# Kernel optimization log

Hardware: AMD Instinct MI355X
Metric: run time of the kernel (lower is better)

## Reference

```python
import jax, jax.numpy as jnp
import numpy as np

# Performer config (from module __init__):
# dim=768, depth=4, heads=12, dim_head=64, nb_features=64,
# generalized_attention=True with ReLU kernel, reversible=True,
# ff_mult=4, shift_tokens=True (shifts=(-1,0,1) since causal=False),
# qkv_bias=True, attn_out_bias=True, ff_chunks=1, dropout=0.
L, D, H, DH, M = 4, 768, 12, 64, 64
FF = 4 * D
SHIFTS = (-1, 0, 1)
KERNEL_EPS = 1e-3


def _layer_norm(x, g, b, eps=1e-5):
    mu = jnp.mean(x, axis=-1, keepdims=True)
    var = jnp.mean((x - mu) ** 2, axis=-1, keepdims=True)
    return (x - mu) / jnp.sqrt(var + eps) * g + b


def _shift(t, amount, mask=None):
    # F.pad(t, (0,0, amount, -amount)): pad front by amount, trim end (or vice versa)
    if amount == 0:
        return t
    if mask is not None:
        t = jnp.where(mask[..., None], t, jnp.zeros((), t.dtype))
    S = t.shape[1]
    f, bk = max(amount, 0), max(-amount, 0)
    return jnp.pad(t, ((0, 0), (f, bk), (0, 0)))[:, bk:bk + S]


def _shift_tokens(x, mask=None):
    # PreShiftTokens with shifts=(-1,0,1): split channels into 3 chunks, shift each along seq
    n = len(SHIFTS)
    fps = x.shape[-1] // n
    parts = [_shift(x[..., i * fps:(i + 1) * fps], a, mask) for i, a in enumerate(SHIFTS)]
    rest = x[..., n * fps:]
    if rest.shape[-1]:
        parts.append(rest)
    return jnp.concatenate(parts, axis=-1)


def _attn(x, mask, Wq, bq, Wk, bk, Wv, bv, Wo, bo, g, bl, P):
    # PreShiftTokens(mask-aware) -> PreLayerNorm -> SelfAttention (FAVOR+ generalized ReLU kernel)
    x = _shift_tokens(x, mask)
    h = _layer_norm(x, g, bl)
    B, S, _ = h.shape
    heads = lambda t: t.reshape(B, S, H, DH).transpose(0, 2, 1, 3)  # b h s d
    q = heads(h @ Wq + bq)
    k = heads(h @ Wk + bk)
    v = heads(h @ Wv + bv)
    # library semantics: zero v where mask is False (module passes input_ids.eq(0))
    v = jnp.where(mask[:, None, :, None], v, jnp.zeros((), v.dtype))
    dn = DH ** -0.25  # data_normalizer
    qp = jax.nn.relu(jnp.einsum('bhnd,md->bhnm', q * dn, P)) + KERNEL_EPS  # [B,H,S,M]
    kp = jax.nn.relu(jnp.einsum('bhnd,md->bhnm', k * dn, P)) + KERNEL_EPS
    ks = kp.sum(axis=2)                                   # [B,H,M]
    d_inv = 1.0 / jnp.einsum('bhnm,bhm->bhn', qp, ks)     # [B,H,S]
    ctx = jnp.einsum('bhnm,bhnd->bhmd', kp, v)            # [B,H,M,DH]
    out = jnp.einsum('bhmd,bhnm,bhn->bhnd', ctx, qp, d_inv)
    out = out.transpose(0, 2, 1, 3).reshape(B, S, H * DH)
    return out @ Wo + bo


def _ff(x, g, bl, W1, b1, W2, b2):
    # PreShiftTokens (no mask routed to FF) -> PreLayerNorm -> FeedForward (exact GELU)
    x = _shift_tokens(x, None)
    h = _layer_norm(x, g, bl)
    return jax.nn.gelu(h @ W1 + b1, approximate=False) @ W2 + b2


def _forward(x, Wq, bq, Wk, bk, Wv, bv, Wo, bo, ln1_g, ln1_b, W1, b1, W2, b2, ln2_g, ln2_b, proj, input_ids):
    mask = (input_ids == 0)  # structure != 'hi': src_pad_mask = input_ids.eq(0)
    # ReversibleSequence: x -> (x, x); per block: y1 = x1 + attn(x2), y2 = x2 + ff(y1)
    x1, x2 = x, x
    for l in range(L):
        y1 = x1 + _attn(x2, mask, Wq[l], bq[l], Wk[l], bk[l], Wv[l], bv[l],
                        Wo[l], bo[l], ln1_g[l], ln1_b[l], proj[l])
        y2 = x2 + _ff(y1, ln2_g[l], ln2_b[l], W1[l], b1[l], W2[l], b2[l])
        x1, x2 = y1, y2
    return (x1 + x2) * 0.5  # stack(chunk(2)).mean(0)


def setup_inputs() -> dict:
    key = jax.random.key(0)
    ks = jax.random.split(key, 16)
    B, S = 8, 2048
    s = 0.02
    f32 = jnp.float32
    return {
        'x': jax.random.normal(ks[0], (B, S, D), f32),
        'input_ids': jax.random.randint(ks[1], (B, S), 0, 1000, dtype=jnp.int32),
        'Wq': jax.random.normal(ks[2], (L, D, D), f32) * s,
        'bq': jnp.zeros((L, D), f32),
        'Wk': jax.random.normal(ks[3], (L, D, D), f32) * s,
        'bk': jnp.zeros((L, D), f32),
        'Wv': jax.random.normal(ks[4], (L, D, D), f32) * s,
        'bv': jnp.zeros((L, D), f32),
        'Wo': jax.random.normal(ks[5], (L, D, D), f32) * s,
        'bo': jnp.zeros((L, D), f32),
        'ln1_g': jnp.ones((L, D), f32),
        'ln1_b': jnp.zeros((L, D), f32),
        'W1': jax.random.normal(ks[6], (L, D, FF), f32) * s,
        'b1': jnp.zeros((L, FF), f32),
        'W2': jax.random.normal(ks[7], (L, FF, D), f32) * s,
        'b2': jnp.zeros((L, D), f32),
        'ln2_g': jnp.ones((L, D), f32),
        'ln2_b': jnp.zeros((L, D), f32),
        'proj': jax.random.normal(ks[8], (L, M, DH), f32),  # FAVOR+ random projection per layer
    }


def reference(x, Wq, bq, Wk, bk, Wv, bv, Wo, bo, ln1_g, ln1_b, W1, b1, W2, b2, ln2_g, ln2_b, proj, input_ids):
    return _forward(x, Wq, bq, Wk, bk, Wv, bv, Wo, bo, ln1_g, ln1_b,
                    W1, b1, W2, b2, ln2_g, ln2_b, proj, input_ids)
```

## Files before the change

### kernel.cpp

```cpp
#include <hip/hip_runtime.h>
#include <cstdint>
#include <cstddef>

typedef __bf16 bf16_t;
typedef bf16_t bf16x4 __attribute__((ext_vector_type(4)));
typedef bf16_t bf16x8 __attribute__((ext_vector_type(8)));
typedef float  f32x4  __attribute__((ext_vector_type(4)));

#define LAYERS 4
#define DMODEL 768
#define NHEAD  12
#define DHEAD  64
#define MFEAT  64
#define FFDIM  3072
#define BB     8
#define SSEQ   2048
#define BSROWS (BB*SSEQ)
#define QROWS  (BSROWS*NHEAD)
#define FFCHUNK (BSROWS/2)
#define SCH    16
#define SPC    (SSEQ/SCH)
#define NBH    (BB*NHEAD)

__device__ __forceinline__ void gload_lds16(const bf16_t* g, bf16_t* l) {
    __builtin_amdgcn_global_load_lds(
        (const __attribute__((address_space(1))) uint32_t*)g,
        (__attribute__((address_space(3))) uint32_t*)l, 16, 0, 0);
}

__global__ __launch_bounds__(256) void castT_kernel(
    const float* __restrict__ in, bf16_t* __restrict__ out, int K, int N)
{
    __shared__ float t[32][33];
    int kb = blockIdx.x * 32, nb = blockIdx.y * 32;
    int tx = threadIdx.x & 31, ty = threadIdx.x >> 5;
#pragma unroll
    for (int i = 0; i < 32; i += 8)
        t[ty + i][tx] = in[(size_t)(kb + ty + i) * N + nb + tx];
    __syncthreads();
#pragma unroll
    for (int i = 0; i < 32; i += 8)
        out[(size_t)(nb + ty + i) * K + kb + tx] = (bf16_t)t[tx][ty + i];
}

__global__ __launch_bounds__(256) void castP_kernel(
    const float* __restrict__ in, bf16_t* __restrict__ out)
{
    int i = blockIdx.x * 256 + threadIdx.x;
    out[i] = (bf16_t)(in[i] * 0.3535533905932738f);
}

template<bool MASKED>
__global__ __launch_bounds__(256) void shiftln_kernel(
    const float* __restrict__ x, const int* __restrict__ ids,
    const float* __restrict__ g, const float* __restrict__ bl,
    bf16_t* __restrict__ out)
{
    const int r = blockIdx.x;
    const int b = r >> 11;
    const int s = r & 2047;
    const int tid = threadIdx.x;
    float v0, v1, v2;
    {
        int s2 = s + 1;
        bool ok = (s2 < SSEQ) && (!MASKED || ids[b * SSEQ + s2] == 0);
        v0 = ok ? x[((size_t)(b * SSEQ + s2)) * DMODEL + tid] : 0.f;
    }
    v1 = x[((size_t)r) * DMODEL + tid + 256];
    {
        int s2 = s - 1;
        bool ok = (s2 >= 0) && (!MASKED || ids[b * SSEQ + s2] == 0);
        v2 = ok ? x[((size_t)(b * SSEQ + s2)) * DMODEL + tid + 512] : 0.f;
    }
    float sum = v0 + v1 + v2;
    float sq  = v0 * v0 + v1 * v1 + v2 * v2;
#pragma unroll
    for (int off = 32; off; off >>= 1) {
        sum += __shfl_down(sum, off);
        sq  += __shfl_down(sq, off);
    }
    __shared__ float red[2][4];
    int lane = tid & 63, w = tid >> 6;
    if (lane == 0) { red[0][w] = sum; red[1][w] = sq; }
    __syncthreads();
    sum = red[0][0] + red[0][1] + red[0][2] + red[0][3];
    sq  = red[1][0] + red[1][1] + red[1][2] + red[1][3];
    float mu  = sum * (1.f / DMODEL);
    float var = sq * (1.f / DMODEL) - mu * mu;
    float rstd = rsqrtf(var + 1e-5f);
    size_t base = (size_t)r * DMODEL;
    out[base + tid]       = (bf16_t)((v0 - mu) * rstd * g[tid]       + bl[tid]);
    out[base + tid + 256] = (bf16_t)((v1 - mu) * rstd * g[tid + 256] + bl[tid + 256]);
    out[base + tid + 512] = (bf16_t)((v2 - mu) * rstd * g[tid + 512] + bl[tid + 512]);
}

template<int BM, int BN, int EPI>
__global__ __launch_bounds__(256) void gemm_kernel(
    const bf16_t* __restrict__ A, const bf16_t* __restrict__ Bt,
    const float* __restrict__ bias, const float* resid,
    const int* __restrict__ ids, void* outp,
    int N, int K)
{
    constexpr int BK = 32;
    constexpr int WM = BM / 2, WN = BN / 2;
    constexpr int AM = WM / 16, AN = WN / 16;
    __shared__ bf16_t As[BM * BK];
    __shared__ bf16_t Bs[BN * BK];
    const int tid  = threadIdx.x;
    const int lane = tid & 63, wid = tid >> 6;
    const int wr = wid >> 1, wc = wid & 1;
    const int rowBase = blockIdx.y * BM;
    const int colBase = blockIdx.x * BN;

    f32x4 acc[AM][AN];
#pragma unroll
    for (int i = 0; i < AM; i++)
#pragma unroll
        for (int j = 0; j < AN; j++) { f32x4 z = {0.f,0.f,0.f,0.f}; acc[i][j] = z; }

    const int krow = (lane >> 4) * 8;
    const int rl   = lane & 15;

    for (int k0 = 0; k0 < K; k0 += BK) {
        __syncthreads();
#pragma unroll
        for (int i = 0; i < (BM * BK) / (256 * 8); i++) {
            int idx = i * 256 + tid;
            int row = idx >> 2, col = (idx & 3) * 8;
            gload_lds16(&A[(size_t)(rowBase + row) * K + k0 + col], &As[idx * 8]);
        }
#pragma unroll
        for (int i = 0; i < (BN * BK) / (256 * 8); i++) {
            int idx = i * 256 + tid;
            int row = idx >> 2, col = (idx & 3) * 8;
            gload_lds16(&Bt[(size_t)(colBase + row) * K + k0 + col], &Bs[idx * 8]);
        }
        __syncthreads();
        bf16x8 af[AM], bfr[AN];
#pragma unroll
        for (int i = 0; i < AM; i++)
            af[i] = *(const bf16x8*)&As[(wr * WM + i * 16 + rl) * BK + krow];
#pragma unroll
        for (int j = 0; j < AN; j++)
            bfr[j] = *(const bf16x8*)&Bs[(wc * WN + j * 16 + rl) * BK + krow];
#pragma unroll
        for (int i = 0; i < AM; i++)
#pragma unroll
            for (int j = 0; j < AN; j++)
                acc[i][j] = __builtin_amdgcn_mfma_f32_16x16x32_bf16(
                    af[i], bfr[j], acc[i][j], 0, 0, 0);
    }

#pragma unroll
    for (int i = 0; i < AM; i++)
#pragma unroll
        for (int j = 0; j < AN; j++) {
            int col = colBase + wc * WN + j * 16 + rl;
#pragma unroll
            for (int r4 = 0; r4 < 4; r4++) {
                int row = rowBase + wr * WM + i * 16 + (lane >> 4) * 4 + r4;
                size_t idx = (size_t)row * N + col;
                float v = acc[i][j][r4];
                if constexpr (EPI == 0) {
                    ((bf16_t*)outp)[idx] = (bf16_t)(v + bias[col]);
                } else if constexpr (EPI == 1) {
                    float o = v + bias[col];
                    if (ids[row] != 0) o = 0.f;
                    ((bf16_t*)outp)[idx] = (bf16_t)o;
                } else if constexpr (EPI == 2) {
                    float o = v > 0.f ? v : 0.f;
                    ((bf16_t*)outp)[idx] = (bf16_t)(o + 0.001f);
                } else if constexpr (EPI == 3) {
                    float xg = v + bias[col];
                    float o = 0.5f * xg * (1.f + erff(xg * 0.70710678118654752f));
                    ((bf16_t*)outp)[idx] = (bf16_t)o;
                } else {
                    ((float*)outp)[idx] = v + bias[col] + resid[idx];
                }
            }
        }
}

__global__ __launch_bounds__(256) void ctx_partial_kernel(
    const bf16_t* __restrict__ kp, const bf16_t* __restrict__ v,
    float* __restrict__ part, float* __restrict__ ksp)
{
    const int blk = blockIdx.x;
    const int bh = blk / SCH, chunk = blk % SCH;
    const int b = bh / NHEAD, h = bh % NHEAD;
    __shared__ float kpf[SPC][64];
    __shared__ float vf[SPC][64];
    const int tid = threadIdx.x;
#pragma unroll
    for (int i = 0; i < 4; i++) {
        int idx = tid + i * 256;
        int sl = idx >> 3, c = (idx & 7) * 8;
        size_t go = ((size_t)(b * SSEQ + chunk * SPC + sl) * NHEAD + h) * 64 + c;
        bf16x8 kv8 = *(const bf16x8*)&kp[go];
        bf16x8 vv8 = *(const bf16x8*)&v[go];
#pragma unroll
        for (int e = 0; e < 8; e++) {
            kpf[sl][c + e] = (float)kv8[e];
            vf[sl][c + e]  = (float)vv8[e];
        }
    }
    __syncthreads();
    const int m = tid & 63, dg = tid >> 6;
    float ksacc = 0.f;
    f32x4 acc[4];
#pragma unroll
    for (int jg = 0; jg < 4; jg++) { f32x4 z = {0.f,0.f,0.f,0.f}; acc[jg] = z; }
    for (int sl = 0; sl < SPC; sl++) {
        float kv = kpf[sl][m];
        ksacc += kv;
#pragma unroll
        for (int jg = 0; jg < 4; jg++) {
            f32x4 c4 = *(const f32x4*)&vf[sl][dg * 16 + jg * 4];
            acc[jg] += kv * c4;
        }
    }
    size_t obase = ((size_t)chunk * NBH + bh) * 4096 + (size_t)m * 64 + dg * 16;
#pragma unroll
    for (int jg = 0; jg < 4; jg++)
#pragma unroll
        for (int e = 0; e < 4; e++) part[obase + jg * 4 + e] = acc[jg][e];
    if (dg == 0) ksp[((size_t)chunk * NBH + bh) * 64 + m] = ksacc;
}

__global__ __launch_bounds__(256) void ctx_reduce_kernel(
    const float* __restrict__ part, float* __restrict__ ctxb)
{
    int e = blockIdx.x * 256 + threadIdx.x;
    float s = 0.f;
#pragma unroll
    for (int c = 0; c < SCH; c++) s += part[(size_t)c * NBH * 4096 + e];
    ctxb[e] = s;
}

__global__ __launch_bounds__(256) void attnout_kernel(
    const bf16_t* __restrict__ qp, const float* __restrict__ ctx,
    const float* __restrict__ ksp, bf16_t* __restrict__ out)
{
    const int blk = blockIdx.x;
    const int sc = blk & 31;
    const int bh = blk >> 5;
    const int b = bh / NHEAD, h = bh % NHEAD;
    __shared__ float ctxs[64][64];
    __shared__ float kss[64];
    const int tid = threadIdx.x;
#pragma unroll
    for (int i = 0; i < 16; i++) {
        int flat = tid + i * 256;
        ctxs[flat >> 6][flat & 63] = ctx[(size_t)bh * 4096 + flat];
    }
    if (tid < 64) {
        float s = 0.f;
#pragma unroll
        for (int c = 0; c < SCH; c++) s += ksp[((size_t)c * NBH + bh) * 64 + tid];
        kss[tid] = s;
    }
    __syncthreads();
    const int sl = tid >> 2, dg = tid & 3;
    const int s = sc * 64 + sl;
    const bf16_t* qrow = &qp[((size_t)(b * SSEQ + s) * NHEAD + h) * 64];
    float den = 0.f;
    f32x4 acc[4];
#pragma unroll
    for (int jg = 0; jg < 4; jg++) { f32x4 z = {0.f,0.f,0.f,0.f}; acc[jg] = z; }
#pragma unroll 4
    for (int m = 0; m < 64; m++) {
        float qv = (float)qrow[m];
        den += qv * kss[m];
#pragma unroll
        for (int jg = 0; jg < 4; jg++) {
            f32x4 c4 = *(const f32x4*)&ctxs[m][dg * 16 + jg * 4];
            acc[jg] += qv * c4;
        }
    }
    float inv = 1.f / den;
    size_t obase = (size_t)(b * SSEQ + s) * DMODEL + h * 64 + dg * 16;
#pragma unroll
    for (int jg = 0; jg < 4; jg++)
#pragma unroll
        for (int e = 0; e < 4; e++)
            out[obase + jg * 4 + e] = (bf16_t)(acc[jg][e] * inv);
}

__global__ void avg_kernel(const float* __restrict__ a, const float* __restrict__ b,
                           float* __restrict__ o, int n4)
{
    for (int i = blockIdx.x * 256 + threadIdx.x; i < n4; i += gridDim.x * 256) {
        f32x4 av = ((const f32x4*)a)[i];
        f32x4 bv = ((const f32x4*)b)[i];
        ((f32x4*)o)[i] = (av + bv) * 0.5f;
    }
}

extern "C" void kernel_launch(void* const* d_in, const int* in_sizes, int n_in,
                              void* d_out, int out_size, void* d_ws, size_t ws_size,
                              hipStream_t stream)
{
    int idi = 1, base = 2;
    if (in_sizes[1] != BSROWS) { idi = n_in - 1; base = 1; }
    const float* x_f   = (const float*)d_in[0];
    const int*   ids   = (const int*)d_in[idi];
    const float* Wq    = (const float*)d_in[base + 0];
    const float* bq    = (const float*)d_in[base + 1];
    const float* Wk    = (const float*)d_in[base + 2];
    const float* bk    = (const float*)d_in[base + 3];
    const float* Wv    = (const float*)d_in[base + 4];
    const float* bv    = (const float*)d_in[base + 5];
    const float* Wo    = (const float*)d_in[base + 6];
    const float* bo    = (const float*)d_in[base + 7];
    const float* ln1g  = (const float*)d_in[base + 8];
    const float* ln1b  = (const float*)d_in[base + 9];
    const float* W1    = (const float*)d_in[base + 10];
    const float* b1    = (const float*)d_in[base + 11];
    const float* W2    = (const float*)d_in[base + 12];
    const float* b2    = (const float*)d_in[base + 13];
    const float* ln2g  = (const float*)d_in[base + 14];
    const float* ln2b  = (const float*)d_in[base + 15];
    const float* proj  = (const float*)d_in[base + 16];

    char* p = (char*)d_ws;
    auto alloc = [&](size_t bytes) -> char* {
        char* r = p; p += (bytes + 255) & ~(size_t)255; return r;
    };
    float*  r1   = (float*)d_out;
    float*  r2   = (float*)alloc((size_t)BSROWS * DMODEL * 4);
    bf16_t* hbuf = (bf16_t*)alloc((size_t)BSROWS * DMODEL * 2);
    char*   ub   = alloc((size_t)3 * BSROWS * DMODEL * 2);
    bf16_t* qb   = (bf16_t*)ub;
    bf16_t* kb   = (bf16_t*)(ub + (size_t)BSROWS * DMODEL * 2);
    bf16_t* vb   = (bf16_t*)(ub + (size_t)2 * BSROWS * DMODEL * 2);
    bf16_t* gff  = (bf16_t*)ub;
    float*  ctxb = (float*)alloc((size_t)NBH * 64 * 64 * 4);
    float*  ksp  = (float*)alloc((size_t)SCH * NBH * 64 * 4);
    char*   wu   = alloc((size_t)2 * DMODEL * FFDIM * 2);
    bf16_t* wqt  = (bf16_t*)wu;
    bf16_t* wkt  = (bf16_t*)(wu + (size_t)DMODEL * DMODEL * 2);
    bf16_t* wvt  = (bf16_t*)(wu + (size_t)2 * DMODEL * DMODEL * 2);
    bf16_t* wot  = (bf16_t*)(wu + (size_t)3 * DMODEL * DMODEL * 2);
    bf16_t* w1t  = (bf16_t*)wu;
    bf16_t* w2t  = (bf16_t*)(wu + (size_t)DMODEL * FFDIM * 2);
    bf16_t* pb   = (bf16_t*)alloc((size_t)MFEAT * DHEAD * 2);
    float*  ctxpart = (float*)hbuf;

    const float* c1 = x_f;
    const float* c2 = x_f;

    for (int l = 0; l < LAYERS; l++) {
        castT_kernel<<<dim3(24, 24), 256, 0, stream>>>(Wq + (size_t)l * DMODEL * DMODEL, wqt, DMODEL, DMODEL);
        castT_kernel<<<dim3(24, 24), 256, 0, stream>>>(Wk + (size_t)l * DMODEL * DMODEL, wkt, DMODEL, DMODEL);
        castT_kernel<<<dim3(24, 24), 256, 0, stream>>>(Wv + (size_t)l * DMODEL * DMODEL, wvt, DMODEL, DMODEL);
        castT_kernel<<<dim3(24, 24), 256, 0, stream>>>(Wo + (size_t)l * DMODEL * DMODEL, wot, DMODEL, DMODEL);
        castP_kernel<<<16, 256, 0, stream>>>(proj + (size_t)l * MFEAT * DHEAD, pb);

        shiftln_kernel<true><<<BSROWS, 256, 0, stream>>>(
            c2, ids, ln1g + l * DMODEL, ln1b + l * DMODEL, hbuf);
        gemm_kernel<128, 128, 0><<<dim3(DMODEL / 128, BSROWS / 128), 256, 0, stream>>>(
            hbuf, wqt, bq + l * DMODEL, nullptr, nullptr, qb, DMODEL, DMODEL);
        gemm_kernel<128, 128, 0><<<dim3(DMODEL / 128, BSROWS / 128), 256, 0, stream>>>(
            hbuf, wkt, bk + l * DMODEL, nullptr, nullptr, kb, DMODEL, DMODEL);
        gemm_kernel<128, 128, 1><<<dim3(DMODEL / 128, BSROWS / 128), 256, 0, stream>>>(
            hbuf, wvt, bv + l * DMODEL, nullptr, ids, vb, DMODEL, DMODEL);
        gemm_kernel<128, 64, 2><<<dim3(1, QROWS / 128), 256, 0, stream>>>(
            qb, pb, nullptr, nullptr, nullptr, qb, MFEAT, DHEAD);
        gemm_kernel<128, 64, 2><<<dim3(1, QROWS / 128), 256, 0, stream>>>(
            kb, pb, nullptr, nullptr, nullptr, kb, MFEAT, DHEAD);
        ctx_partial_kernel<<<NBH * SCH, 256, 0, stream>>>(kb, vb, ctxpart, ksp);
        ctx_reduce_kernel<<<(NBH * 4096) / 256, 256, 0, stream>>>(ctxpart, ctxb);
        attnout_kernel<<<NBH * (SSEQ / 64), 256, 0, stream>>>(qb, ctxb, ksp, hbuf);
        gemm_kernel<128, 128, 4><<<dim3(DMODEL / 128, BSROWS / 128), 256, 0, stream>>>(
            hbuf, wot, bo + l * DMODEL, c1, nullptr, r1, DMODEL, DMODEL);
        c1 = r1;

        castT_kernel<<<dim3(24, 96), 256, 0, stream>>>(W1 + (size_t)l * DMODEL * FFDIM, w1t, DMODEL, FFDIM);
        castT_kernel<<<dim3(96, 24), 256, 0, stream>>>(W2 + (size_t)l * FFDIM * DMODEL, w2t, FFDIM, DMODEL);

        shiftln_kernel<false><<<BSROWS, 256, 0, stream>>>(
            c1, ids, ln2g + l * DMODEL, ln2b + l * DMODEL, hbuf);
        for (int ch = 0; ch < 2; ch++) {
            const bf16_t* hA = hbuf + (size_t)ch * FFCHUNK * DMODEL;
            gemm_kernel<128, 128, 3><<<dim3(FFDIM / 128, FFCHUNK / 128), 256, 0, stream>>>(
                hA, w1t, b1 + l * FFDIM, nullptr, nullptr, gff, FFDIM, DMODEL);
            gemm_kernel<128, 128, 4><<<dim3(DMODEL / 128, FFCHUNK / 128), 256, 0, stream>>>(
                gff, w2t, b2 + l * DMODEL, c2 + (size_t)ch * FFCHUNK * DMODEL, nullptr,
                r2 + (size_t)ch * FFCHUNK * DMODEL, DMODEL, FFDIM);
        }
        c2 = r2;
    }

    avg_kernel<<<4096, 256, 0, stream>>>(c1, c2, (float*)d_out,
                                         (BSROWS * DMODEL) / 4);
}
```

Before: 2.730 ms.

## Fuse QKV GEMMs, widen K tile with swizzled LDS, remap workgroups

Merges the three Q/K/V projection GEMMs into one N=2304 GEMM whose epilogue writes into the separate q/k/v buffers, using a concatenated bias and masking only the V third. The GEMM kernel also doubles BK to 64 with an XOR-swizzled LDS layout to avoid bank conflicts, halving the barriers per K step. Workgroup IDs are remapped to spread consecutive blocks across XCDs. Aims to cut launch overhead, re-reads of the LN output, and LDS stalls, at the cost of more shared memory per block. The projection GEMM with K=64 now runs as one iteration.

Measured after the change: 2.565 ms. 1.06x faster.

```diff
diff --git a/kernel.cpp b/kernel.cpp
--- a/kernel.cpp
+++ b/kernel.cpp
@@ -50,6 +50,18 @@
     out[i] = (bf16_t)(in[i] * 0.3535533905932738f);
 }
 
+__global__ __launch_bounds__(256) void biascat_kernel(
+    const float* __restrict__ bq, const float* __restrict__ bk,
+    const float* __restrict__ bv, float* __restrict__ out)
+{
+    int i = blockIdx.x * 256 + threadIdx.x;
+    int l = i / 2304, j = i % 2304;
+    float v = (j < 768) ? bq[l * 768 + j]
+            : (j < 1536) ? bk[l * 768 + j - 768]
+                         : bv[l * 768 + j - 1536];
+    out[i] = v;
+}
+
 template<bool MASKED>
 __global__ __launch_bounds__(256) void shiftln_kernel(
     const float* __restrict__ x, const int* __restrict__ ids,
@@ -101,7 +113,7 @@
     const int* __restrict__ ids, void* outp,
     int N, int K)
 {
-    constexpr int BK = 32;
+    constexpr int BK = 64;
     constexpr int WM = BM / 2, WN = BN / 2;
     constexpr int AM = WM / 16, AN = WN / 16;
     __shared__ bf16_t As[BM * BK];
@@ -109,8 +121,13 @@
     const int tid  = threadIdx.x;
     const int lane = tid & 63, wid = tid >> 6;
     const int wr = wid >> 1, wc = wid & 1;
-    const int rowBase = blockIdx.y * BM;
-    const int colBase = blockIdx.x * BN;
+    const int gx = gridDim.x;
+    const int nwg = gx * (int)gridDim.y;
+    int orig = (int)blockIdx.y * gx + (int)blockIdx.x;
+    int wgid = orig;
+    if ((nwg & 7) == 0) wgid = (orig & 7) * (nwg >> 3) + (orig >> 3);
+    const int rowBase = (wgid / gx) * BM;
+    const int colBase = (wgid % gx) * BN;
 
     f32x4 acc[AM][AN];
 #pragma unroll
@@ -118,37 +135,47 @@
 #pragma unroll
         for (int j = 0; j < AN; j++) { f32x4 z = {0.f,0.f,0.f,0.f}; acc[i][j] = z; }
 
-    const int krow = (lane >> 4) * 8;
-    const int rl   = lane & 15;
+    const int rl = lane & 15;
+    const int c0 = lane >> 4;
+    const int sx = rl & 7;
 
     for (int k0 = 0; k0 < K; k0 += BK) {
         __syncthreads();
 #pragma unroll
-        for (int i = 0; i < (BM * BK) / (256 * 8); i++) {
+        for (int i = 0; i < (BM * 8) / 256; i++) {
             int idx = i * 256 + tid;
-            int row = idx >> 2, col = (idx & 3) * 8;
-            gload_lds16(&A[(size_t)(rowBase + row) * K + k0 + col], &As[idx * 8]);
-        }
-#pragma unroll
-        for (int i = 0; i < (BN * BK) / (256 * 8); i++) {
+            int row = idx >> 3, ccp = idx & 7;
+            int ccl = ccp ^ (row & 7);
+            gload_lds16(&A[(size_t)(rowBase + row) * K + k0 + ccl * 8], &As[idx * 8]);
+        }
+#pragma unroll
+        for (int i = 0; i < (BN * 8) / 256; i++) {
             int idx = i * 256 + tid;
-            int row = idx >> 2, col = (idx & 3) * 8;
-            gload_lds16(&Bt[(size_t)(colBase + row) * K + k0 + col], &Bs[idx * 8]);
+            int row = idx >> 3, ccp = idx & 7;
+            int ccl = ccp ^ (row & 7);
+            gload_lds16(&Bt[(size_t)(colBase + row) * K + k0 + ccl * 8], &Bs[idx * 8]);
         }
         __syncthreads();
-        bf16x8 af[AM], bfr[AN];
-#pragma unroll
-        for (int i = 0; i < AM; i++)
-            af[i] = *(const bf16x8*)&As[(wr * WM + i * 16 + rl) * BK + krow];
-#pragma unroll
-        for (int j = 0; j < AN; j++)
-            bfr[j] = *(const bf16x8*)&Bs[(wc * WN + j * 16 + rl) * BK + krow];
-#pragma unroll
-        for (int i = 0; i < AM; i++)
-#pragma unroll
-            for (int j = 0; j < AN; j++)
-                acc[i][j] = __builtin_amdgcn_mfma_f32_16x16x32_bf16(
-                    af[i], bfr[j], acc[i][j], 0, 0, 0);
+#pragma unroll
+        for (int kk = 0; kk < 2; kk++) {
+            bf16x8 af[AM], bfr[AN];
+#pragma unroll
+            for (int i = 0; i < AM; i++) {
+                int ccp = ((kk << 2) | c0) ^ sx;
+                af[i] = *(const bf16x8*)&As[(wr * WM + i * 16 + rl) * BK + ccp * 8];
+            }
+#pragma unroll
+            for (int j = 0; j < AN; j++) {
+                int ccp = ((kk << 2) | c0) ^ sx;
+                bfr[j] = *(const bf16x8*)&Bs[(wc * WN + j * 16 + rl) * BK + ccp * 8];
+            }
+#pragma unroll
+            for (int i = 0; i < AM; i++)
+#pragma unroll
+                for (int j = 0; j < AN; j++)
+                    acc[i][j] = __builtin_amdgcn_mfma_f32_16x16x32_bf16(
+                        af[i], bfr[j], acc[i][j], 0, 0, 0);
+        }
     }
 
 #pragma unroll
@@ -159,23 +186,24 @@
 #pragma unroll
             for (int r4 = 0; r4 < 4; r4++) {
                 int row = rowBase + wr * WM + i * 16 + (lane >> 4) * 4 + r4;
-                size_t idx = (size_t)row * N + col;
                 float v = acc[i][j][r4];
-                if constexpr (EPI == 0) {
-                    ((bf16_t*)outp)[idx] = (bf16_t)(v + bias[col]);
-                } else if constexpr (EPI == 1) {
-                    float o = v + bias[col];
-                    if (ids[row] != 0) o = 0.f;
-                    ((bf16_t*)outp)[idx] = (bf16_t)o;
-                } else if constexpr (EPI == 2) {
+                if constexpr (EPI == 2) {
                     float o = v > 0.f ? v : 0.f;
-                    ((bf16_t*)outp)[idx] = (bf16_t)(o + 0.001f);
+                    ((bf16_t*)outp)[(size_t)row * N + col] = (bf16_t)(o + 0.001f);
                 } else if constexpr (EPI == 3) {
                     float xg = v + bias[col];
                     float o = 0.5f * xg * (1.f + erff(xg * 0.70710678118654752f));
-                    ((bf16_t*)outp)[idx] = (bf16_t)o;
+                    ((bf16_t*)outp)[(size_t)row * N + col] = (bf16_t)o;
+                } else if constexpr (EPI == 4) {
+                    size_t idx = (size_t)row * N + col;
+                    ((float*)outp)[idx] = v + bias[col] + resid[idx];
                 } else {
-                    ((float*)outp)[idx] = v + bias[col] + resid[idx];
+                    int third = col / DMODEL;
+                    int colq  = col - third * DMODEL;
+                    float o = v + bias[col];
+                    if (third == 2 && ids[row] != 0) o = 0.f;
+                    bf16_t* ob = (bf16_t*)outp + (size_t)third * BSROWS * DMODEL;
+                    ob[(size_t)row * DMODEL + colq] = (bf16_t)o;
                 }
             }
         }
@@ -337,33 +365,30 @@
     float*  ctxb = (float*)alloc((size_t)NBH * 64 * 64 * 4);
     float*  ksp  = (float*)alloc((size_t)SCH * NBH * 64 * 4);
     char*   wu   = alloc((size_t)2 * DMODEL * FFDIM * 2);
-    bf16_t* wqt  = (bf16_t*)wu;
-    bf16_t* wkt  = (bf16_t*)(wu + (size_t)DMODEL * DMODEL * 2);
-    bf16_t* wvt  = (bf16_t*)(wu + (size_t)2 * DMODEL * DMODEL * 2);
+    bf16_t* wqkvt = (bf16_t*)wu;
     bf16_t* wot  = (bf16_t*)(wu + (size_t)3 * DMODEL * DMODEL * 2);
     bf16_t* w1t  = (bf16_t*)wu;
     bf16_t* w2t  = (bf16_t*)(wu + (size_t)DMODEL * FFDIM * 2);
     bf16_t* pb   = (bf16_t*)alloc((size_t)MFEAT * DHEAD * 2);
+    float*  bqkv = (float*)alloc((size_t)LAYERS * 2304 * 4);
     float*  ctxpart = (float*)hbuf;
+
+    biascat_kernel<<<(LAYERS * 2304) / 256, 256, 0, stream>>>(bq, bk, bv, bqkv);
 
     const float* c1 = x_f;
     const float* c2 = x_f;
 
     for (int l = 0; l < LAYERS; l++) {
-        castT_kernel<<<dim3(24, 24), 256, 0, stream>>>(Wq + (size_t)l * DMODEL * DMODEL, wqt, DMODEL, DMODEL);
-        castT_kernel<<<dim3(24, 24), 256, 0, stream>>>(Wk + (size_t)l * DMODEL * DMODEL, wkt, DMODEL, DMODEL);
-        castT_kernel<<<dim3(24, 24), 256, 0, stream>>>(Wv + (size_t)l * DMODEL * DMODEL, wvt, DMODEL, DMODEL);
+        castT_kernel<<<dim3(24, 24), 256, 0, stream>>>(Wq + (size_t)l * DMODEL * DMODEL, wqkvt, DMODEL, DMODEL);
+        castT_kernel<<<dim3(24, 24), 256, 0, stream>>>(Wk + (size_t)l * DMODEL * DMODEL, wqkvt + (size_t)DMODEL * DMODEL, DMODEL, DMODEL);
+        castT_kernel<<<dim3(24, 24), 256, 0, stream>>>(Wv + (size_t)l * DMODEL * DMODEL, wqkvt + (size_t)2 * DMODEL * DMODEL, DMODEL, DMODEL);
         castT_kernel<<<dim3(24, 24), 256, 0, stream>>>(Wo + (size_t)l * DMODEL * DMODEL, wot, DMODEL, DMODEL);
         castP_kernel<<<16, 256, 0, stream>>>(proj + (size_t)l * MFEAT * DHEAD, pb);
 
         shiftln_kernel<true><<<BSROWS, 256, 0, stream>>>(
             c2, ids, ln1g + l * DMODEL, ln1b + l * DMODEL, hbuf);
-        gemm_kernel<128, 128, 0><<<dim3(DMODEL / 128, BSROWS / 128), 256, 0, stream>>>(
-            hbuf, wqt, bq + l * DMODEL, nullptr, nullptr, qb, DMODEL, DMODEL);
-        gemm_kernel<128, 128, 0><<<dim3(DMODEL / 128, BSROWS / 128), 256, 0, stream>>>(
-            hbuf, wkt, bk + l * DMODEL, nullptr, nullptr, kb, DMODEL, DMODEL);
-        gemm_kernel<128, 128, 1><<<dim3(DMODEL / 128, BSROWS / 128), 256, 0, stream>>>(
-            hbuf, wvt, bv + l * DMODEL, nullptr, ids, vb, DMODEL, DMODEL);
+        gemm_kernel<128, 128, 5><<<dim3(2304 / 128, BSROWS / 128), 256, 0, stream>>>(
+            hbuf, wqkvt, bqkv + l * 2304, nullptr, ids, qb, 2304, DMODEL);
         gemm_kernel<128, 64, 2><<<dim3(1, QROWS / 128), 256, 0, stream>>>(
             qb, pb, nullptr, nullptr, nullptr, qb, MFEAT, DHEAD);
         gemm_kernel<128, 64, 2><<<dim3(1, QROWS / 128), 256, 0, stream>>>(
```
